# Optimization experiments

Hardware: AMD Instinct MI355X
Metric: run time of the kernel (lower is better)

The kernel has to match this reference:

```python
import jax, jax.numpy as jnp
import numpy as np

B, C_IN, C_OUT, K, H, W, STRIDE, PAD = 64, 64, 128, 3, 32, 32, 1, 1
H_OUT = (H + 2 * PAD - K) // STRIDE + 1
W_OUT = (W + 2 * PAD - K) // STRIDE + 1


def setup_inputs() -> dict:
    key = jax.random.key(0)
    k1, k2 = jax.random.split(key)
    x = jax.random.normal(k1, (B, C_IN, H, W), dtype=jnp.float32)
    fan_in = C_IN * K * K
    weight = jax.random.normal(k2, (C_OUT, H_OUT, W_OUT, C_IN, K, K), dtype=jnp.float32) / np.sqrt(fan_in).astype(np.float32)
    bias = jnp.zeros((C_OUT, H_OUT, W_OUT), dtype=jnp.float32)
    return {"x": x, "weight": weight, "bias": bias}


def _extract_patches(x):
    # x: [B, C, H, W] -> patches [B, C, H_OUT, W_OUT, K, K]
    xp = jnp.pad(x, ((0, 0), (0, 0), (PAD, PAD), (PAD, PAD)))
    rows = []
    for k in range(K):  # small fixed kernel loop (K=3), not a data-dim loop
        cols = []
        for l in range(K):
            cols.append(xp[:, :, k:k + H_OUT * STRIDE:STRIDE, l:l + W_OUT * STRIDE:STRIDE])
        rows.append(jnp.stack(cols, axis=-1))
    return jnp.stack(rows, axis=-2)


def reference(x, weight, bias):
    patches = _extract_patches(x)  # [B, C_IN, H_OUT, W_OUT, K, K]
    # per-location unshared GEMM: out[b,o,h,w] = sum_{i,k,l} weight[o,h,w,i,k,l] * patches[b,i,h,w,k,l]
    out = jnp.einsum('ohwikl,bihwkl->bohw', weight, patches)
    return out + bias[None]
```

## Files before the change

### kernel.cpp

```cpp
#include <hip/hip_runtime.h>


typedef __bf16  bf16x8  __attribute__((ext_vector_type(8)));
typedef float   floatx4 __attribute__((ext_vector_type(4)));

static __device__ inline bf16x8 cvt8(floatx4 a, floatx4 b) {
    bf16x8 r;
    r[0] = (__bf16)a[0]; r[1] = (__bf16)a[1]; r[2] = (__bf16)a[2]; r[3] = (__bf16)a[3];
    r[4] = (__bf16)b[0]; r[5] = (__bf16)b[1]; r[6] = (__bf16)b[2]; r[7] = (__bf16)b[3];
    return r;
}

__global__ __launch_bounds__(256, 3) void prep_kernel(
    const float* __restrict__ x, __bf16* __restrict__ P)
{
    __shared__ float xl[16 * 772];

    const int tid = threadIdx.x;
    const int bid = blockIdx.x;
    const int bq = bid & 3;
    const int ig = (bid >> 2) & 7;
    const int h  = bid >> 5;

    #pragma unroll
    for (int it = 0; it < 12; ++it) {
        int g   = tid + (it << 8);
        int row = g >> 3;
        int sub = g & 7;
        int bl  = row / 24;
        int rem = row - bl * 24;
        int il  = rem / 3;
        int ky  = rem - il * 3;
        int y   = h + ky - 1;
        floatx4 v = {0.f, 0.f, 0.f, 0.f};
        if ((unsigned)y < 32u) {
            const float* src = x + (((size_t)(bq * 16 + bl) * 64 + ig * 8 + il) << 10)
                                 + y * 32 + (sub << 2);
            v = *(const floatx4*)src;
        }
        *(floatx4*)&xl[bl * 772 + il * 96 + ky * 32 + (sub << 2)] = v;
    }
    __syncthreads();

    const int lane = tid & 63;
    const int wv = tid >> 6;
    const int bl = lane & 15;
    const int qq = lane >> 4;

    #pragma unroll 2
    for (int it = 0; it < 18; ++it) {
        int pr  = (it << 4) + (wv << 2) + qq;
        int w   = pr / 9;
        int kol = pr - w * 9;
        int ko  = ig * 9 + kol;
        bf16x8 piece;
        #pragma unroll
        for (int j = 0; j < 8; ++j) {
            int klocal = (kol << 3) + j;
            int il = klocal / 9;
            int p  = klocal - il * 9;
            int ky = p / 3;
            int kx = p - ky * 3;
            int xc = w + kx - 1;
            float v = ((unsigned)xc < 32u) ? xl[bl * 772 + il * 96 + ky * 32 + xc] : 0.0f;
            piece[j] = (__bf16)v;
        }
        int loc   = (h << 5) + w;
        int idx16 = ((ko >> 2) << 8) + (bq << 6) + ((ko & 3) << 4) + bl;
        *(bf16x8*)&P[((size_t)loc * 4608 + idx16) * 8] = piece;
    }
}

__global__ __launch_bounds__(256, 3) void local2d_kernel(
    const __bf16* __restrict__ P,
    const float* __restrict__ weight,
    const float* __restrict__ bias,
    float* __restrict__ out)
{
    __shared__ __bf16 alds[6 * 4 * 64 * 8];
    __shared__ __bf16 wlds[24 * 65 * 8];

    const int tid  = threadIdx.x;
    const int lane = tid & 63;
    const int wv   = tid >> 6;
    const int ll   = lane & 15;
    const int q    = lane >> 4;

    const int bid = blockIdx.x;
    const int xcd = bid & 7;
    const int og  = (bid >> 3) & 1;
    const int w   = (bid >> 4) & 31;
    const int hl  = bid >> 9;
    const int h   = (xcd << 2) + hl;
    const int loc = (h << 5) + w;

    const __bf16* Ploc  = P + (size_t)loc * 36864;
    const float*  wbase = weight + ((size_t)(og << 6) * 1024 + loc) * 576;

    floatx4 acc[4];
    #pragma unroll
    for (int nt = 0; nt < 4; ++nt) acc[nt] = (floatx4){0.f, 0.f, 0.f, 0.f};

    for (int c = 0; c < 3; ++c) {
        #pragma unroll
        for (int it = 0; it < 6; ++it) {
            const __bf16* g = Ploc + c * 12288 + ((((it << 2) + wv) << 6) | lane) * 8;
            __builtin_amdgcn_global_load_lds(
                (const __attribute__((address_space(1))) unsigned int*)g,
                (__attribute__((address_space(3))) unsigned int*)&alds[(((it << 2) + wv) << 6) * 8],
                16, 0, 0);
        }
        #pragma unroll
        for (int it = 0; it < 6; ++it) {
            int g  = tid + (it << 8);
            int ol = g / 24;
            int jg = g - ol * 24;
            const float* src = wbase + (size_t)ol * 589824 + c * 192 + (jg << 3);
            floatx4 va = *(const floatx4*)src;
            floatx4 vb = *(const floatx4*)(src + 4);
            int t  = jg >> 2;
            int qw = jg & 3;
            int nt = ol >> 4;
            int lw = ol & 15;
            *(bf16x8*)&wlds[(((t << 2) + nt) * 65 + (qw << 4) + lw) * 8] = cvt8(va, vb);
        }
        __syncthreads();

        #pragma unroll
        for (int t = 0; t < 6; ++t) {
            bf16x8 af = *(const bf16x8*)&alds[((((t << 2) + wv) << 6) | lane) * 8];
            #pragma unroll
            for (int nt = 0; nt < 4; ++nt) {
                bf16x8 bw = *(const bf16x8*)&wlds[(((t << 2) + nt) * 65 + lane) * 8];
                acc[nt] = __builtin_amdgcn_mfma_f32_16x16x32_bf16(af, bw, acc[nt], 0, 0, 0);
            }
        }
        __syncthreads();
    }

    #pragma unroll
    for (int nt = 0; nt < 4; ++nt) {
        int o = (og << 6) + (nt << 4) + ll;
        float bv = bias[((size_t)o << 10) + loc];
        #pragma unroll
        for (int r = 0; r < 4; ++r) {
            int m = (wv << 4) + (q << 2) + r;
            out[(((size_t)m << 7) + o) * 1024 + loc] = acc[nt][r] + bv;
        }
    }
}

extern "C" void kernel_launch(void* const* d_in, const int* in_sizes, int n_in,
                              void* d_out, int out_size, void* d_ws, size_t ws_size,
                              hipStream_t stream) {
    const float* x  = (const float*)d_in[0];
    const float* wt = (const float*)d_in[1];
    const float* bi = (const float*)d_in[2];
    float* out = (float*)d_out;
    __bf16* P = (__bf16*)d_ws;
    prep_kernel<<<dim3(1024), dim3(256), 0, stream>>>(x, P);
    local2d_kernel<<<dim3(2048), dim3(256), 0, stream>>>(P, wt, bi, out);
}
```

Baseline: 507.2 us.

## Load weights directly into MFMA registers, cover all output channels per block

The local2d kernel now handles all 128 output channels per block, with half as many blocks, so each patch tile is fetched once instead of twice. Weight fragments are read straight from global memory into registers and converted to bf16 per MFMA, which removes the weight LDS staging and its barriers. The patch tiles use an LDS double buffer so the next chunk's load overlaps compute. In exchange, every wave now loads all weights redundantly, register pressure grows, and there are fewer blocks to hide latency.

```diff
diff --git a/kernel.cpp b/kernel.cpp
--- a/kernel.cpp
+++ b/kernel.cpp
@@ -77,8 +77,7 @@
     const float* __restrict__ bias,
     float* __restrict__ out)
 {
-    __shared__ __bf16 alds[6 * 4 * 64 * 8];
-    __shared__ __bf16 wlds[24 * 65 * 8];
+    __shared__ __bf16 alds[2][12288];
 
     const int tid  = threadIdx.x;
     const int lane = tid & 63;
@@ -88,59 +87,61 @@
 
     const int bid = blockIdx.x;
     const int xcd = bid & 7;
-    const int og  = (bid >> 3) & 1;
-    const int w   = (bid >> 4) & 31;
-    const int hl  = bid >> 9;
+    const int w   = (bid >> 3) & 31;
+    const int hl  = bid >> 8;
     const int h   = (xcd << 2) + hl;
     const int loc = (h << 5) + w;
 
-    const __bf16* Ploc  = P + (size_t)loc * 36864;
-    const float*  wbase = weight + ((size_t)(og << 6) * 1024 + loc) * 576;
+    const __bf16* Ploc = P + (size_t)loc * 36864;
 
-    floatx4 acc[4];
+    const float* wlane = weight + ((size_t)ll * 1024 + loc) * 576 + (q << 3);
+    const float* wptr[8];
     #pragma unroll
-    for (int nt = 0; nt < 4; ++nt) acc[nt] = (floatx4){0.f, 0.f, 0.f, 0.f};
+    for (int nt = 0; nt < 8; ++nt) wptr[nt] = wlane + (size_t)nt * 9437184;
 
+    floatx4 acc[8];
+    #pragma unroll
+    for (int nt = 0; nt < 8; ++nt) acc[nt] = (floatx4){0.f, 0.f, 0.f, 0.f};
+
+    #pragma unroll
+    for (int it = 0; it < 6; ++it) {
+        const __bf16* g = Ploc + ((((it << 2) + wv) << 6) | lane) * 8;
+        __builtin_amdgcn_global_load_lds(
+            (const __attribute__((address_space(1))) unsigned int*)g,
+            (__attribute__((address_space(3))) unsigned int*)&alds[0][(((it << 2) + wv) << 6) * 8],
+            16, 0, 0);
+    }
+    __syncthreads();
+
+    #pragma unroll
     for (int c = 0; c < 3; ++c) {
-        #pragma unroll
-        for (int it = 0; it < 6; ++it) {
-            const __bf16* g = Ploc + c * 12288 + ((((it << 2) + wv) << 6) | lane) * 8;
-            __builtin_amdgcn_global_load_lds(
-                (const __attribute__((address_space(1))) unsigned int*)g,
-                (__attribute__((address_space(3))) unsigned int*)&alds[(((it << 2) + wv) << 6) * 8],
-                16, 0, 0);
+        if (c < 2) {
+            #pragma unroll
+            for (int it = 0; it < 6; ++it) {
+                const __bf16* g = Ploc + (c + 1) * 12288 + ((((it << 2) + wv) << 6) | lane) * 8;
+                __builtin_amdgcn_global_load_lds(
+                    (const __attribute__((address_space(1))) unsigned int*)g,
+                    (__attribute__((address_space(3))) unsigned int*)&alds[(c + 1) & 1][(((it << 2) + wv) << 6) * 8],
+                    16, 0, 0);
+            }
         }
         #pragma unroll
-        for (int it = 0; it < 6; ++it) {
-            int g  = tid + (it << 8);
-            int ol = g / 24;
-            int jg = g - ol * 24;
-            const float* src = wbase + (size_t)ol * 589824 + c * 192 + (jg << 3);
-            floatx4 va = *(const floatx4*)src;
-            floatx4 vb = *(const floatx4*)(src + 4);
-            int t  = jg >> 2;
-            int qw = jg & 3;
-            int nt = ol >> 4;
-            int lw = ol & 15;
-            *(bf16x8*)&wlds[(((t << 2) + nt) * 65 + (qw << 4) + lw) * 8] = cvt8(va, vb);
-        }
-        __syncthreads();
-
-        #pragma unroll
         for (int t = 0; t < 6; ++t) {
-            bf16x8 af = *(const bf16x8*)&alds[((((t << 2) + wv) << 6) | lane) * 8];
+            bf16x8 af = *(const bf16x8*)&alds[c & 1][((((t << 2) + wv) << 6) | lane) * 8];
             #pragma unroll
-            for (int nt = 0; nt < 4; ++nt) {
-                bf16x8 bw = *(const bf16x8*)&wlds[(((t << 2) + nt) * 65 + lane) * 8];
-                acc[nt] = __builtin_amdgcn_mfma_f32_16x16x32_bf16(af, bw, acc[nt], 0, 0, 0);
+            for (int nt = 0; nt < 8; ++nt) {
+                const float* src = wptr[nt] + c * 192 + t * 32;
+                floatx4 va = *(const floatx4*)src;
+                floatx4 vb = *(const floatx4*)(src + 4);
+                acc[nt] = __builtin_amdgcn_mfma_f32_16x16x32_bf16(af, cvt8(va, vb), acc[nt], 0, 0, 0);
             }
         }
-        __syncthreads();
+        if (c < 2) __syncthreads();
     }
 
     #pragma unroll
-    for (int nt = 0; nt < 4; ++nt) {
-        int o = (og << 6) + (nt << 4) + ll;
+    for (int nt = 0; nt < 8; ++nt) {
+        int o = (nt << 4) + ll;
         float bv = bias[((size_t)o << 10) + loc];
         #pragma unroll
         for (int r = 0; r < 4; ++r) {
@@ -159,5 +160,5 @@
     float* out = (float*)d_out;
     __bf16* P = (__bf16*)d_ws;
     prep_kernel<<<dim3(1024), dim3(256), 0, stream>>>(x, P);
-    local2d_kernel<<<dim3(2048), dim3(256), 0, stream>>>(P, wt, bi, out);
+    local2d_kernel<<<dim3(1024), dim3(256), 0, stream>>>(P, wt, bi, out);
 }
```

Result: slower. 547.2 us (+7.9%).
